# Kernel tuning notes

Hardware: AMD Instinct MI355X
Metric: run time of the kernel (lower is better)

## Reference

```python
import jax, jax.numpy as jnp
import numpy as np

WS = 7        # window_size
HEADS = 3
HEAD_DIM = 32


def _relative_indices(ws):
    idx = np.array([[x, y] for x in range(ws) for y in range(ws)])  # [ws*ws, 2]
    dist = idx[None, :, :] - idx[:, None, :]
    dist[:, :, 0] += ws - 1
    dist[:, :, 1] += ws - 1
    dist[:, :, 0] *= 2 * ws - 1
    return jnp.asarray(dist.sum(-1))  # [ws*ws, ws*ws] int


_REL_IDX = _relative_indices(WS)


def setup_inputs() -> dict:
    key = jax.random.key(0)
    k1, k2, k3, k4, k5 = jax.random.split(key, 5)
    dim = 96
    inner = HEADS * HEAD_DIM  # 96
    return {
        "x": jax.random.normal(k1, (64, dim, 56, 56), dtype=jnp.float32),
        "w_qkv": jax.random.normal(k2, (dim, inner * 3), dtype=jnp.float32) * 0.05,
        "pos_emb": jax.random.normal(k3, ((2 * WS - 1) ** 2, HEADS), dtype=jnp.float32),
        "w_out": jax.random.normal(k4, (inner, dim), dtype=jnp.float32) * 0.05,
        "b_out": jax.random.normal(k5, (dim,), dtype=jnp.float32),
    }


def _to_windows(t, b, H, W, ws, h, d):
    # [b, H, W, h*d] -> [b, h, nw_h*nw_w, ws*ws, d]  (non-shuffle layout)
    nwh, nww = H // ws, W // ws
    t = t.reshape(b, nwh, ws, nww, ws, h, d)
    t = t.transpose(0, 5, 1, 3, 2, 4, 6)  # b h nwh nww wh ww d
    return t.reshape(b, h, nwh * nww, ws * ws, d)


def reference(x, w_qkv, pos_emb, w_out, b_out):
    ws, h, d = WS, HEADS, HEAD_DIM
    scale = d ** (-0.5)
    x = x.transpose(0, 2, 3, 1)  # b, H, W, c
    b, H, W, _ = x.shape
    nwh, nww = H // ws, W // ws
    qkv = x @ w_qkv  # b, H, W, 3*inner
    q, k, v = jnp.split(qkv, 3, axis=-1)
    q = _to_windows(q, b, H, W, ws, h, d)
    k = _to_windows(k, b, H, W, ws, h, d)
    v = _to_windows(v, b, H, W, ws, h, d)
    dots = jnp.einsum('bhwid,bhwjd->bhwij', q, k) * scale
    # relative position bias: gather [ws*ws, ws*ws, heads] -> [1, h, 1, i, j]
    bias = pos_emb[_REL_IDX]  # [ws*ws, ws*ws, h]
    dots = dots + bias.transpose(2, 0, 1)[None, :, None]
    attn = jax.nn.softmax(dots, axis=-1)
    out = jnp.einsum('bhwij,bhwjd->bhwid', attn, v)  # b h nw ws*ws d
    out = out.reshape(b, h, nwh, nww, ws, ws, d)
    out = out.transpose(0, 2, 4, 3, 5, 1, 6).reshape(b, H, W, h * d)
    out = out @ w_out + b_out
    return out.transpose(0, 3, 1, 2)  # b, dim, H, W
```

## Files before the change

kernel.cpp:

```cpp
#include <hip/hip_runtime.h>

typedef __bf16 bf16;
typedef __bf16 bf16x4 __attribute__((ext_vector_type(4)));
typedef __bf16 bf16x8 __attribute__((ext_vector_type(8)));
typedef float  f32x4  __attribute__((ext_vector_type(4)));

#define SCALE 0.17677669529663687f
#define LOG2E 1.4426950408889634f

#define WQKVT_OFF 0
#define WOUTT_OFF 55296
#define BIASC_OFF 73728

#define CBAR() asm volatile("" ::: "memory")

template <int CTRL>
__device__ __forceinline__ float dpp_mv(float x) {
    return __int_as_float(__builtin_amdgcn_update_dpp(
        0, __float_as_int(x), CTRL, 0xF, 0xF, true));
}
__device__ __forceinline__ float row16_max(float m) {
    m = fmaxf(m, dpp_mv<0xB1>(m));
    m = fmaxf(m, dpp_mv<0x4E>(m));
    m = fmaxf(m, dpp_mv<0x124>(m));
    m = fmaxf(m, dpp_mv<0x128>(m));
    return m;
}
__device__ __forceinline__ float row16_sum(float s) {
    s += dpp_mv<0xB1>(s);
    s += dpp_mv<0x4E>(s);
    s += dpp_mv<0x124>(s);
    s += dpp_mv<0x128>(s);
    return s;
}

__global__ __launch_bounds__(512)
void prep(const float* __restrict__ wqkv, const float* __restrict__ pos,
          const float* __restrict__ wout, bf16* __restrict__ wqkvT,
          bf16* __restrict__ woutT, float* __restrict__ biasC)
{
    int tid = blockIdx.x * 512 + threadIdx.x;
    const int stride = 4 * 512;
    for (int i = tid; i < 288 * 96; i += stride) {
        int n = i / 96, c = i % 96;
        float v = wqkv[c * 288 + n];
        if (n < 96) v *= SCALE * LOG2E;
        wqkvT[i] = (bf16)v;
    }
    for (int i = tid; i < 96 * 96; i += stride) {
        int o = i / 96, c = i % 96;
        woutT[i] = (bf16)wout[c * 96 + o];
    }
    for (int i = tid; i < 3 * 4 * 4 * 64 * 4; i += stride) {
        int e = i & 3, lane = (i >> 2) & 63, wv = (i >> 8) & 3, ni = (i >> 10) & 3, h = i >> 12;
        int row = wv * 16 + ((lane >> 4) << 2) + e;
        int col = ni * 16 + (lane & 15);
        float v;
        if (col >= 49) v = -1e30f;
        else if (row >= 49) v = 0.f;
        else {
            int ridx = ((col / 7) - (row / 7) + 6) * 13 + ((col % 7) - (row % 7) + 6);
            v = pos[ridx * 3 + h] * LOG2E;
        }
        biasC[i] = v;
    }
}

__global__ __launch_bounds__(256, 4)
void winattn(const float* __restrict__ x, const float* __restrict__ bout,
             const bf16* __restrict__ wqkvT, const bf16* __restrict__ woutT,
             const float* __restrict__ biasC, float* __restrict__ out)
{
    __shared__ __align__(16) unsigned char smem[40448];
    bf16* qall = (bf16*)(smem);
    bf16* kall = (bf16*)(smem + 13312);
    bf16* vt   = (bf16*)(smem + 26624);
    bf16* xs   = (bf16*)(smem + 26624);
    bf16* Ost  = (bf16*)(smem);
    float* fin = (float*)(smem + 13312);

    const int tid = threadIdx.x;
    const int w = tid >> 6, lane = tid & 63;
    const int lr = lane & 15, lk = lane >> 4;

    const int blkraw = blockIdx.x;
    const int b  = blkraw >> 6;
    const int wh = blkraw & 7;
    const int ww = (blkraw >> 3) & 7;
    const int row0 = wh * 7, col0 = ww * 7;

    {
        const int t = lane;
        const int c0 = w * 24;
        const bool valid = t < 49;
        const int tr = valid ? t / 7 : 0, tc = valid ? t % 7 : 0;
        const float* xp = x + ((size_t)(b * 96 + c0)) * 3136
                            + (row0 + tr) * 56 + col0 + tc;
        bf16* xw = &xs[t * 108 + c0];
#pragma unroll
        for (int j = 0; j < 24; ++j) {
            float v = xp[(size_t)j * 3136];
            xw[j] = (bf16)(valid ? v : 0.f);
        }
    }
    __syncthreads();

    bf16x8 a[4][3];
#pragma unroll
    for (int mi = 0; mi < 4; ++mi)
#pragma unroll
        for (int k = 0; k < 3; ++k) {
            bf16x4 lo = *(const bf16x4*)&xs[(mi * 16 + lr) * 108 + k * 32 + lk * 8];
            bf16x4 hi = *(const bf16x4*)&xs[(mi * 16 + lr) * 108 + k * 32 + lk * 8 + 4];
            a[mi][k] = __builtin_shufflevector(lo, hi, 0, 1, 2, 3, 4, 5, 6, 7);
        }
    __syncthreads();

    {
        auto compute = [&](int ni, f32x4 (&acc)[4]) {
#pragma unroll
            for (int mi = 0; mi < 4; ++mi) acc[mi] = (f32x4){0.f, 0.f, 0.f, 0.f};
#pragma unroll
            for (int k = 0; k < 3; ++k) {
                bf16x8 bb = *(const bf16x8*)&wqkvT[(ni * 16 + lr) * 96 + k * 32 + lk * 8];
#pragma unroll
                for (int mi = 0; mi < 4; ++mi)
                    acc[mi] = __builtin_amdgcn_mfma_f32_16x16x32_bf16(a[mi][k], bb, acc[mi], 0, 0, 0);
            }
        };
        auto writeQ = [&](int ni, f32x4 (&acc)[4]) {
#pragma unroll
            for (int mi = 0; mi < 4; ++mi)
#pragma unroll
                for (int e = 0; e < 4; ++e)
                    qall[(mi * 16 + lk * 4 + e) * 104 + ni * 16 + lr] = (bf16)acc[mi][e];
        };
        auto writeK = [&](int ni, f32x4 (&acc)[4]) {
#pragma unroll
            for (int mi = 0; mi < 4; ++mi)
#pragma unroll
                for (int e = 0; e < 4; ++e)
                    kall[(mi * 16 + lk * 4 + e) * 104 + (ni - 6) * 16 + lr] = (bf16)acc[mi][e];
        };
        auto writeV = [&](int ni, f32x4 (&acc)[4]) {
#pragma unroll
            for (int mi = 0; mi < 4; ++mi) {
                bf16x4 pk;
#pragma unroll
                for (int e = 0; e < 4; ++e) pk[e] = (bf16)acc[mi][e];
                *(bf16x4*)&vt[((ni - 12) * 16 + lr) * 72 + mi * 16 + lk * 4] = pk;
            }
        };

        f32x4 acc[4];
        compute(w, acc);       writeQ(w, acc);
        compute(w + 4, acc);   if (w < 2) writeQ(w + 4, acc); else writeK(w + 4, acc);
        compute(w + 8, acc);   writeK(w + 8, acc);
        compute(w + 12, acc);  writeV(w + 12, acc);
        if (w < 2) { compute(w + 16, acc); writeV(w + 16, acc); }
    }
    f32x4 bias0[4], bias1[4], bias2[4];
#pragma unroll
    for (int ni = 0; ni < 4; ++ni)
        bias0[ni] = *(const f32x4*)&biasC[(size_t)((0 * 4 + ni) * 4 + w) * 256 + lane * 4];
    __syncthreads();

    bf16x8 qa[3];
#pragma unroll
    for (int h = 0; h < 3; ++h)
        qa[h] = *(const bf16x8*)&qall[(w * 16 + lr) * 104 + h * 32 + lk * 8];
    CBAR();

    bf16* Pw = (bf16*)(smem + w * 3328);

    f32x4 oacc[3][2];
#pragma unroll
    for (int h = 0; h < 3; ++h)
#pragma unroll
        for (int ni = 0; ni < 2; ++ni) oacc[h][ni] = (f32x4){0.f, 0.f, 0.f, 0.f};

#pragma unroll
    for (int h = 0; h < 3; ++h) {
        f32x4 sacc[4];
        const f32x4* bc = (h == 0) ? bias0 : (h == 1) ? bias1 : bias2;
#pragma unroll
        for (int ni = 0; ni < 4; ++ni) {
            bf16x8 kb = *(const bf16x8*)&kall[(ni * 16 + lr) * 104 + h * 32 + lk * 8];
            sacc[ni] = __builtin_amdgcn_mfma_f32_16x16x32_bf16(qa[h], kb, bc[ni], 0, 0, 0);
        }
        if (h == 0) {
#pragma unroll
            for (int ni = 0; ni < 4; ++ni)
                bias1[ni] = *(const f32x4*)&biasC[(size_t)((1 * 4 + ni) * 4 + w) * 256 + lane * 4];
        } else if (h == 1) {
#pragma unroll
            for (int ni = 0; ni < 4; ++ni)
                bias2[ni] = *(const f32x4*)&biasC[(size_t)((2 * 4 + ni) * 4 + w) * 256 + lane * 4];
        }
#pragma unroll
        for (int e = 0; e < 4; ++e) {
            float s0 = sacc[0][e], s1 = sacc[1][e], s2 = sacc[2][e], s3 = sacc[3][e];
            float m = row16_max(fmaxf(fmaxf(s0, s1), fmaxf(s2, s3)));
            float p0 = exp2f(s0 - m), p1 = exp2f(s1 - m);
            float p2 = exp2f(s2 - m), p3 = exp2f(s3 - m);
            float s = row16_sum((p0 + p1) + (p2 + p3));
            float inv = __builtin_amdgcn_rcpf(s);
            int rl = lk * 4 + e;
            Pw[rl * 72 + lr]      = (bf16)(p0 * inv);
            Pw[rl * 72 + 16 + lr] = (bf16)(p1 * inv);
            Pw[rl * 72 + 32 + lr] = (bf16)(p2 * inv);
            Pw[rl * 72 + 48 + lr] = (bf16)(p3 * inv);
        }
        CBAR();
#pragma unroll
        for (int kk = 0; kk < 2; ++kk) {
            bf16x8 pa = *(const bf16x8*)&Pw[lr * 72 + kk * 32 + lk * 8];
#pragma unroll
            for (int ni = 0; ni < 2; ++ni) {
                bf16x8 vb = *(const bf16x8*)&vt[(h * 32 + ni * 16 + lr) * 72 + kk * 32 + lk * 8];
                oacc[h][ni] = __builtin_amdgcn_mfma_f32_16x16x32_bf16(pa, vb, oacc[h][ni], 0, 0, 0);
            }
        }
        CBAR();
    }

#pragma unroll
    for (int h = 0; h < 3; ++h)
#pragma unroll
        for (int ni = 0; ni < 2; ++ni)
#pragma unroll
            for (int e = 0; e < 4; ++e)
                Ost[(w * 16 + lk * 4 + e) * 104 + h * 32 + ni * 16 + lr]
                    = (bf16)oacc[h][ni][e];
    __syncthreads();

    {
        const int pcnt = (w < 2) ? 2 : 1;
#pragma unroll
        for (int j = 0; j < 2; ++j) {
            if (j < pcnt) {
                const int ni = w + j * 4;
                const float bo = bout[ni * 16 + lr];
                f32x4 pacc[4];
#pragma unroll
                for (int mi = 0; mi < 4; ++mi) pacc[mi] = (f32x4){0.f, 0.f, 0.f, 0.f};
#pragma unroll
                for (int k = 0; k < 3; ++k) {
                    bf16x8 wb = *(const bf16x8*)&woutT[(ni * 16 + lr) * 96 + k * 32 + lk * 8];
#pragma unroll
                    for (int mi = 0; mi < 4; ++mi) {
                        bf16x8 as = *(const bf16x8*)&Ost[(mi * 16 + lr) * 104 + k * 32 + lk * 8];
                        pacc[mi] = __builtin_amdgcn_mfma_f32_16x16x32_bf16(as, wb, pacc[mi], 0, 0, 0);
                    }
                }
#pragma unroll
                for (int mi = 0; mi < 4; ++mi)
#pragma unroll
                    for (int e = 0; e < 4; ++e)
                        fin[(mi * 16 + lk * 4 + e) * 101 + ni * 16 + lr] = pacc[mi][e] + bo;
            }
        }
    }
    __syncthreads();

    {
        const int t = lane;
        if (t < 49) {
            const int off = (row0 + t / 7) * 56 + col0 + t % 7;
            float* ob = out + (size_t)(b * 96 + w * 24) * 3136 + off;
            const float* fr = fin + t * 101 + w * 24;
#pragma unroll
            for (int j = 0; j < 24; ++j)
                ob[(size_t)j * 3136] = fr[j];
        }
    }
}

extern "C" void kernel_launch(void* const* d_in, const int* in_sizes, int n_in,
                              void* d_out, int out_size, void* d_ws, size_t ws_size,
                              hipStream_t stream) {
    const float* x    = (const float*)d_in[0];
    const float* wqkv = (const float*)d_in[1];
    const float* pos  = (const float*)d_in[2];
    const float* wout = (const float*)d_in[3];
    const float* bout = (const float*)d_in[4];
    float* outp = (float*)d_out;

    bf16*  wqkvT = (bf16*)((char*)d_ws + WQKVT_OFF);
    bf16*  woutT = (bf16*)((char*)d_ws + WOUTT_OFF);
    float* biasC = (float*)((char*)d_ws + BIASC_OFF);

    prep<<<dim3(4), dim3(512), 0, stream>>>(wqkv, pos, wout, wqkvT, woutT, biasC);
    winattn<<<dim3(4096), dim3(256), 0, stream>>>(x, bout, wqkvT, woutT,
                                                  biasC, outp);
}
```

Baseline: 80.02 us.

## Process four windows per block and prefetch next window's input during writeback

Each block now loops over four horizontally adjacent windows instead of handling one. The shared-memory layout is rearranged so the next window's input tile can be staged into the A region while the current window's output is read from the B region and stored. The aim is to amortize block launch and setup cost and to overlap global loads with stores. In exchange the grid shrinks from 4096 to 1024 blocks, which lowers parallelism and may leave CUs underfilled.

```diff
diff --git a/kernel.cpp b/kernel.cpp
--- a/kernel.cpp
+++ b/kernel.cpp
@@ -13,6 +13,10 @@
 #define BIASC_OFF 73728
 
 #define CBAR() asm volatile("" ::: "memory")
+
+#define REG_A 0
+#define REG_B 13824
+#define REG_C 27136
 
 template <int CTRL>
 __device__ __forceinline__ float dpp_mv(float x) {
@@ -71,25 +75,26 @@
              const bf16* __restrict__ wqkvT, const bf16* __restrict__ woutT,
              const float* __restrict__ biasC, float* __restrict__ out)
 {
-    __shared__ __align__(16) unsigned char smem[40448];
-    bf16* qall = (bf16*)(smem);
-    bf16* kall = (bf16*)(smem + 13312);
-    bf16* vt   = (bf16*)(smem + 26624);
-    bf16* xs   = (bf16*)(smem + 26624);
-    bf16* Ost  = (bf16*)(smem);
-    float* fin = (float*)(smem + 13312);
+    __shared__ __align__(16) unsigned char smem[40960];
+    bf16* xs   = (bf16*)(smem + REG_A);
+    bf16* qall = (bf16*)(smem + REG_A);
+    bf16* Ost  = (bf16*)(smem + REG_A);
+    bf16* kall = (bf16*)(smem + REG_B);
+    bf16* vt   = (bf16*)(smem + REG_C);
+    float* fin = (float*)(smem + REG_B);
 
     const int tid = threadIdx.x;
     const int w = tid >> 6, lane = tid & 63;
     const int lr = lane & 15, lk = lane >> 4;
 
     const int blkraw = blockIdx.x;
-    const int b  = blkraw >> 6;
+    const int b  = blkraw >> 4;
     const int wh = blkraw & 7;
-    const int ww = (blkraw >> 3) & 7;
-    const int row0 = wh * 7, col0 = ww * 7;
-
-    {
+    const int wg = (blkraw >> 3) & 1;
+    const int row0 = wh * 7;
+
+    auto stage = [&](int ww) {
+        const int col0 = ww * 7;
         const int t = lane;
         const int c0 = w * 24;
         const bool valid = t < 49;
@@ -102,176 +107,184 @@
             float v = xp[(size_t)j * 3136];
             xw[j] = (bf16)(valid ? v : 0.f);
         }
-    }
-    __syncthreads();
-
-    bf16x8 a[4][3];
-#pragma unroll
-    for (int mi = 0; mi < 4; ++mi)
-#pragma unroll
-        for (int k = 0; k < 3; ++k) {
-            bf16x4 lo = *(const bf16x4*)&xs[(mi * 16 + lr) * 108 + k * 32 + lk * 8];
-            bf16x4 hi = *(const bf16x4*)&xs[(mi * 16 + lr) * 108 + k * 32 + lk * 8 + 4];
-            a[mi][k] = __builtin_shufflevector(lo, hi, 0, 1, 2, 3, 4, 5, 6, 7);
-        }
-    __syncthreads();
-
-    {
-        auto compute = [&](int ni, f32x4 (&acc)[4]) {
-#pragma unroll
-            for (int mi = 0; mi < 4; ++mi) acc[mi] = (f32x4){0.f, 0.f, 0.f, 0.f};
+    };
+
+    stage(wg * 4);
+
+    for (int wi = 0; wi < 4; ++wi) {
+        const int ww = wg * 4 + wi;
+        const int col0 = ww * 7;
+        __syncthreads();
+
+        bf16x8 a[4][3];
+#pragma unroll
+        for (int mi = 0; mi < 4; ++mi)
 #pragma unroll
             for (int k = 0; k < 3; ++k) {
-                bf16x8 bb = *(const bf16x8*)&wqkvT[(ni * 16 + lr) * 96 + k * 32 + lk * 8];
+                bf16x4 lo = *(const bf16x4*)&xs[(mi * 16 + lr) * 108 + k * 32 + lk * 8];
+                bf16x4 hi = *(const bf16x4*)&xs[(mi * 16 + lr) * 108 + k * 32 + lk * 8 + 4];
+                a[mi][k] = __builtin_shufflevector(lo, hi, 0, 1, 2, 3, 4, 5, 6, 7);
+            }
+        __syncthreads();
+
+        {
+            auto compute = [&](int ni, f32x4 (&acc)[4]) {
+#pragma unroll
+                for (int mi = 0; mi < 4; ++mi) acc[mi] = (f32x4){0.f, 0.f, 0.f, 0.f};
+#pragma unroll
+                for (int k = 0; k < 3; ++k) {
+                    bf16x8 bb = *(const bf16x8*)&wqkvT[(ni * 16 + lr) * 96 + k * 32 + lk * 8];
+#pragma unroll
+                    for (int mi = 0; mi < 4; ++mi)
+                        acc[mi] = __builtin_amdgcn_mfma_f32_16x16x32_bf16(a[mi][k], bb, acc[mi], 0, 0, 0);
+                }
+            };
+            auto writeQ = [&](int ni, f32x4 (&acc)[4]) {
 #pragma unroll
                 for (int mi = 0; mi < 4; ++mi)
-                    acc[mi] = __builtin_amdgcn_mfma_f32_16x16x32_bf16(a[mi][k], bb, acc[mi], 0, 0, 0);
-            }
-        };
-        auto writeQ = [&](int ni, f32x4 (&acc)[4]) {
-#pragma unroll
-            for (int mi = 0; mi < 4; ++mi)
+#pragma unroll
+                    for (int e = 0; e < 4; ++e)
+                        qall[(mi * 16 + lk * 4 + e) * 104 + ni * 16 + lr] = (bf16)acc[mi][e];
+            };
+            auto writeK = [&](int ni, f32x4 (&acc)[4]) {
+#pragma unroll
+                for (int mi = 0; mi < 4; ++mi)
+#pragma unroll
+                    for (int e = 0; e < 4; ++e)
+                        kall[(mi * 16 + lk * 4 + e) * 104 + (ni - 6) * 16 + lr] = (bf16)acc[mi][e];
+            };
+            auto writeV = [&](int ni, f32x4 (&acc)[4]) {
+#pragma unroll
+                for (int mi = 0; mi < 4; ++mi) {
+                    bf16x4 pk;
+#pragma unroll
+                    for (int e = 0; e < 4; ++e) pk[e] = (bf16)acc[mi][e];
+                    *(bf16x4*)&vt[((ni - 12) * 16 + lr) * 72 + mi * 16 + lk * 4] = pk;
+                }
+            };
+
+            f32x4 acc[4];
+            compute(w, acc);       writeQ(w, acc);
+            compute(w + 4, acc);   if (w < 2) writeQ(w + 4, acc); else writeK(w + 4, acc);
+            compute(w + 8, acc);   writeK(w + 8, acc);
+            compute(w + 12, acc);  writeV(w + 12, acc);
+            if (w < 2) { compute(w + 16, acc); writeV(w + 16, acc); }
+        }
+        f32x4 bias0[4], bias1[4], bias2[4];
+#pragma unroll
+        for (int ni = 0; ni < 4; ++ni)
+            bias0[ni] = *(const f32x4*)&biasC[(size_t)((0 * 4 + ni) * 4 + w) * 256 + lane * 4];
+        __syncthreads();
+
+        bf16x8 qa[3];
+#pragma unroll
+        for (int h = 0; h < 3; ++h)
+            qa[h] = *(const bf16x8*)&qall[(w * 16 + lr) * 104 + h * 32 + lk * 8];
+        CBAR();
+
+        bf16* Pw = (bf16*)(smem + REG_A + w * 3328);
+
+        f32x4 oacc[3][2];
+#pragma unroll
+        for (int h = 0; h < 3; ++h)
+#pragma unroll
+            for (int ni = 0; ni < 2; ++ni) oacc[h][ni] = (f32x4){0.f, 0.f, 0.f, 0.f};
+
+#pragma unroll
+        for (int h = 0; h < 3; ++h) {
+            f32x4 sacc[4];
+            const f32x4* bc = (h == 0) ? bias0 : (h == 1) ? bias1 : bias2;
+#pragma unroll
+            for (int ni = 0; ni < 4; ++ni) {
+                bf16x8 kb = *(const bf16x8*)&kall[(ni * 16 + lr) * 104 + h * 32 + lk * 8];
+                sacc[ni] = __builtin_amdgcn_mfma_f32_16x16x32_bf16(qa[h], kb, bc[ni], 0, 0, 0);
+            }
+            if (h == 0) {
+#pragma unroll
+                for (int ni = 0; ni < 4; ++ni)
+                    bias1[ni] = *(const f32x4*)&biasC[(size_t)((1 * 4 + ni) * 4 + w) * 256 + lane * 4];
+            } else if (h == 1) {
+#pragma unroll
+                for (int ni = 0; ni < 4; ++ni)
+                    bias2[ni] = *(const f32x4*)&biasC[(size_t)((2 * 4 + ni) * 4 + w) * 256 + lane * 4];
+            }
+#pragma unroll
+            for (int e = 0; e < 4; ++e) {
+                float s0 = sacc[0][e], s1 = sacc[1][e], s2 = sacc[2][e], s3 = sacc[3][e];
+                float m = row16_max(fmaxf(fmaxf(s0, s1), fmaxf(s2, s3)));
+                float p0 = exp2f(s0 - m), p1 = exp2f(s1 - m);
+                float p2 = exp2f(s2 - m), p3 = exp2f(s3 - m);
+                float s = row16_sum((p0 + p1) + (p2 + p3));
+                float inv = __builtin_amdgcn_rcpf(s);
+                int rl = lk * 4 + e;
+                Pw[rl * 72 + lr]      = (bf16)(p0 * inv);
+                Pw[rl * 72 + 16 + lr] = (bf16)(p1 * inv);
+                Pw[rl * 72 + 32 + lr] = (bf16)(p2 * inv);
+                Pw[rl * 72 + 48 + lr] = (bf16)(p3 * inv);
+            }
+            CBAR();
+#pragma unroll
+            for (int kk = 0; kk < 2; ++kk) {
+                bf16x8 pa = *(const bf16x8*)&Pw[lr * 72 + kk * 32 + lk * 8];
+#pragma unroll
+                for (int ni = 0; ni < 2; ++ni) {
+                    bf16x8 vb = *(const bf16x8*)&vt[(h * 32 + ni * 16 + lr) * 72 + kk * 32 + lk * 8];
+                    oacc[h][ni] = __builtin_amdgcn_mfma_f32_16x16x32_bf16(pa, vb, oacc[h][ni], 0, 0, 0);
+                }
+            }
+            CBAR();
+        }
+
+#pragma unroll
+        for (int h = 0; h < 3; ++h)
+#pragma unroll
+            for (int ni = 0; ni < 2; ++ni)
 #pragma unroll
                 for (int e = 0; e < 4; ++e)
-                    qall[(mi * 16 + lk * 4 + e) * 104 + ni * 16 + lr] = (bf16)acc[mi][e];
-        };
-        auto writeK = [&](int ni, f32x4 (&acc)[4]) {
-#pragma unroll
-            for (int mi = 0; mi < 4; ++mi)
-#pragma unroll
-                for (int e = 0; e < 4; ++e)
-                    kall[(mi * 16 + lk * 4 + e) * 104 + (ni - 6) * 16 + lr] = (bf16)acc[mi][e];
-        };
-        auto writeV = [&](int ni, f32x4 (&acc)[4]) {
-#pragma unroll
-            for (int mi = 0; mi < 4; ++mi) {
-                bf16x4 pk;
-#pragma unroll
-                for (int e = 0; e < 4; ++e) pk[e] = (bf16)acc[mi][e];
-                *(bf16x4*)&vt[((ni - 12) * 16 + lr) * 72 + mi * 16 + lk * 4] = pk;
-            }
-        };
-
-        f32x4 acc[4];
-        compute(w, acc);       writeQ(w, acc);
-        compute(w + 4, acc);   if (w < 2) writeQ(w + 4, acc); else writeK(w + 4, acc);
-        compute(w + 8, acc);   writeK(w + 8, acc);
-        compute(w + 12, acc);  writeV(w + 12, acc);
-        if (w < 2) { compute(w + 16, acc); writeV(w + 16, acc); }
-    }
-    f32x4 bias0[4], bias1[4], bias2[4];
-#pragma unroll
-    for (int ni = 0; ni < 4; ++ni)
-        bias0[ni] = *(const f32x4*)&biasC[(size_t)((0 * 4 + ni) * 4 + w) * 256 + lane * 4];
-    __syncthreads();
-
-    bf16x8 qa[3];
-#pragma unroll
-    for (int h = 0; h < 3; ++h)
-        qa[h] = *(const bf16x8*)&qall[(w * 16 + lr) * 104 + h * 32 + lk * 8];
-    CBAR();
-
-    bf16* Pw = (bf16*)(smem + w * 3328);
-
-    f32x4 oacc[3][2];
-#pragma unroll
-    for (int h = 0; h < 3; ++h)
-#pragma unroll
-        for (int ni = 0; ni < 2; ++ni) oacc[h][ni] = (f32x4){0.f, 0.f, 0.f, 0.f};
-
-#pragma unroll
-    for (int h = 0; h < 3; ++h) {
-        f32x4 sacc[4];
-        const f32x4* bc = (h == 0) ? bias0 : (h == 1) ? bias1 : bias2;
-#pragma unroll
-        for (int ni = 0; ni < 4; ++ni) {
-            bf16x8 kb = *(const bf16x8*)&kall[(ni * 16 + lr) * 104 + h * 32 + lk * 8];
-            sacc[ni] = __builtin_amdgcn_mfma_f32_16x16x32_bf16(qa[h], kb, bc[ni], 0, 0, 0);
-        }
-        if (h == 0) {
-#pragma unroll
-            for (int ni = 0; ni < 4; ++ni)
-                bias1[ni] = *(const f32x4*)&biasC[(size_t)((1 * 4 + ni) * 4 + w) * 256 + lane * 4];
-        } else if (h == 1) {
-#pragma unroll
-            for (int ni = 0; ni < 4; ++ni)
-                bias2[ni] = *(const f32x4*)&biasC[(size_t)((2 * 4 + ni) * 4 + w) * 256 + lane * 4];
-        }
-#pragma unroll
-        for (int e = 0; e < 4; ++e) {
-            float s0 = sacc[0][e], s1 = sacc[1][e], s2 = sacc[2][e], s3 = sacc[3][e];
-            float m = row16_max(fmaxf(fmaxf(s0, s1), fmaxf(s2, s3)));
-            float p0 = exp2f(s0 - m), p1 = exp2f(s1 - m);
-            float p2 = exp2f(s2 - m), p3 = exp2f(s3 - m);
-            float s = row16_sum((p0 + p1) + (p2 + p3));
-            float inv = __builtin_amdgcn_rcpf(s);
-            int rl = lk * 4 + e;
-            Pw[rl * 72 + lr]      = (bf16)(p0 * inv);
-            Pw[rl * 72 + 16 + lr] = (bf16)(p1 * inv);
-            Pw[rl * 72 + 32 + lr] = (bf16)(p2 * inv);
-            Pw[rl * 72 + 48 + lr] = (bf16)(p3 * inv);
-        }
-        CBAR();
-#pragma unroll
-        for (int kk = 0; kk < 2; ++kk) {
-            bf16x8 pa = *(const bf16x8*)&Pw[lr * 72 + kk * 32 + lk * 8];
-#pragma unroll
-            for (int ni = 0; ni < 2; ++ni) {
-                bf16x8 vb = *(const bf16x8*)&vt[(h * 32 + ni * 16 + lr) * 72 + kk * 32 + lk * 8];
-                oacc[h][ni] = __builtin_amdgcn_mfma_f32_16x16x32_bf16(pa, vb, oacc[h][ni], 0, 0, 0);
-            }
-        }
-        CBAR();
-    }
-
-#pragma unroll
-    for (int h = 0; h < 3; ++h)
-#pragma unroll
-        for (int ni = 0; ni < 2; ++ni)
-#pragma unroll
-            for (int e = 0; e < 4; ++e)
-                Ost[(w * 16 + lk * 4 + e) * 104 + h * 32 + ni * 16 + lr]
-                    = (bf16)oacc[h][ni][e];
-    __syncthreads();
-
-    {
-        const int pcnt = (w < 2) ? 2 : 1;
-#pragma unroll
-        for (int j = 0; j < 2; ++j) {
-            if (j < pcnt) {
-                const int ni = w + j * 4;
-                const float bo = bout[ni * 16 + lr];
-                f32x4 pacc[4];
-#pragma unroll
-                for (int mi = 0; mi < 4; ++mi) pacc[mi] = (f32x4){0.f, 0.f, 0.f, 0.f};
-#pragma unroll
-                for (int k = 0; k < 3; ++k) {
-                    bf16x8 wb = *(const bf16x8*)&woutT[(ni * 16 + lr) * 96 + k * 32 + lk * 8];
-#pragma unroll
-                    for (int mi = 0; mi < 4; ++mi) {
-                        bf16x8 as = *(const bf16x8*)&Ost[(mi * 16 + lr) * 104 + k * 32 + lk * 8];
-                        pacc[mi] = __builtin_amdgcn_mfma_f32_16x16x32_bf16(as, wb, pacc[mi], 0, 0, 0);
+                    Ost[(w * 16 + lk * 4 + e) * 104 + h * 32 + ni * 16 + lr]
+                        = (bf16)oacc[h][ni][e];
+        __syncthreads();
+
+        {
+            const int pcnt = (w < 2) ? 2 : 1;
+#pragma unroll
+            for (int j = 0; j < 2; ++j) {
+                if (j < pcnt) {
+                    const int ni = w + j * 4;
+                    const float bo = bout[ni * 16 + lr];
+                    f32x4 pacc[4];
+#pragma unroll
+                    for (int mi = 0; mi < 4; ++mi) pacc[mi] = (f32x4){0.f, 0.f, 0.f, 0.f};
+#pragma unroll
+                    for (int k = 0; k < 3; ++k) {
+                        bf16x8 wb = *(const bf16x8*)&woutT[(ni * 16 + lr) * 96 + k * 32 + lk * 8];
+#pragma unroll
+                        for (int mi = 0; mi < 4; ++mi) {
+                            bf16x8 as = *(const bf16x8*)&Ost[(mi * 16 + lr) * 104 + k * 32 + lk * 8];
+                            pacc[mi] = __builtin_amdgcn_mfma_f32_16x16x32_bf16(as, wb, pacc[mi], 0, 0, 0);
+                        }
                     }
+#pragma unroll
+                    for (int mi = 0; mi < 4; ++mi)
+#pragma unroll
+                        for (int e = 0; e < 4; ++e)
+                            fin[(mi * 16 + lk * 4 + e) * 101 + ni * 16 + lr] = pacc[mi][e] + bo;
                 }
-#pragma unroll
-                for (int mi = 0; mi < 4; ++mi)
-#pragma unroll
-                    for (int e = 0; e < 4; ++e)
-                        fin[(mi * 16 + lk * 4 + e) * 101 + ni * 16 + lr] = pacc[mi][e] + bo;
-            }
-        }
-    }
-    __syncthreads();
-
-    {
-        const int t = lane;
-        if (t < 49) {
-            const int off = (row0 + t / 7) * 56 + col0 + t % 7;
-            float* ob = out + (size_t)(b * 96 + w * 24) * 3136 + off;
-            const float* fr = fin + t * 101 + w * 24;
-#pragma unroll
-            for (int j = 0; j < 24; ++j)
-                ob[(size_t)j * 3136] = fr[j];
+            }
+        }
+        __syncthreads();
+
+        if (wi < 3) stage(ww + 1);
+        {
+            const int t = lane;
+            if (t < 49) {
+                const int off = (row0 + t / 7) * 56 + col0 + t % 7;
+                float* ob = out + (size_t)(b * 96 + w * 24) * 3136 + off;
+                const float* fr = fin + t * 101 + w * 24;
+#pragma unroll
+                for (int j = 0; j < 24; ++j)
+                    ob[(size_t)j * 3136] = fr[j];
+            }
         }
     }
 }
@@ -291,6 +304,6 @@
     float* biasC = (float*)((char*)d_ws + BIASC_OFF);
 
     prep<<<dim3(4), dim3(512), 0, stream>>>(wqkv, pos, wout, wqkvT, woutT, biasC);
-    winattn<<<dim3(4096), dim3(256), 0, stream>>>(x, bout, wqkvT, woutT,
+    winattn<<<dim3(1024), dim3(256), 0, stream>>>(x, bout, wqkvT, woutT,
                                                   biasC, outp);
 }
```

Measured after the change: 162.9 us. +103.6%, slower.
